# Kernel optimization log

Measured on AMD Instinct MI355X. Metric: run time of the kernel, lower is better.

## Reference

```python
import jax, jax.numpy as jnp
import numpy as np

C_IN, C_KEY, C_VAL, C_OUT = 256, 128, 128, 256
B, H, W = 4, 64, 64
BN_EPS = 1e-5


def conv1x1(x, w, b):
    # x: [B,C,H,W], w: [O,C], b: [O]
    return jnp.einsum('bchw,oc->bohw', x, w) + b[None, :, None, None]


def bn_relu(x, gamma, beta, mean, var):
    inv = jax.lax.rsqrt(var + BN_EPS)
    y = (x - mean[None, :, None, None]) * (gamma * inv)[None, :, None, None] + beta[None, :, None, None]
    return jax.nn.relu(y)


def setup_inputs() -> dict:
    key = jax.random.key(0)
    ks = jax.random.split(key, 16)
    s = 0.05
    return {
        'x_enc': jax.random.normal(ks[0], (B, C_IN, H, W), jnp.float32),
        'x_dec': jax.random.normal(ks[1], (B, C_IN, H, W), jnp.float32),
        # f_key: conv + BN params
        'wk': jax.random.normal(ks[2], (C_KEY, C_IN), jnp.float32) * s,
        'bk': jax.random.normal(ks[3], (C_KEY,), jnp.float32) * s,
        'gk': jax.random.uniform(ks[4], (C_KEY,), jnp.float32, 0.5, 1.5),
        'betak': jax.random.normal(ks[5], (C_KEY,), jnp.float32) * s,
        'mk': jax.random.normal(ks[6], (C_KEY,), jnp.float32) * s,
        'vk': jax.random.uniform(ks[7], (C_KEY,), jnp.float32, 0.5, 1.5),
        # f_query: conv + BN params
        'wq': jax.random.normal(ks[8], (C_KEY, C_IN), jnp.float32) * s,
        'bq': jax.random.normal(ks[9], (C_KEY,), jnp.float32) * s,
        'gq': jax.random.uniform(ks[10], (C_KEY,), jnp.float32, 0.5, 1.5),
        'betaq': jax.random.normal(ks[11], (C_KEY,), jnp.float32) * s,
        'mq': jax.random.normal(ks[12], (C_KEY,), jnp.float32) * s,
        'vq': jax.random.uniform(ks[13], (C_KEY,), jnp.float32, 0.5, 1.5),
        # f_value conv
        'wv': jax.random.normal(ks[14], (C_VAL, C_IN), jnp.float32) * s,
        'bv': jnp.zeros((C_VAL,), jnp.float32),
        # output projection W (random instead of zero-init to avoid degenerate baseline)
        'wo': jax.random.normal(ks[15], (C_OUT, C_VAL), jnp.float32) * s,
        'bo': jnp.zeros((C_OUT,), jnp.float32),
    }


def reference(x_enc, x_dec, wk, bk, gk, betak, mk, vk, wq, bq, gq, betaq, mq, vq, wv, bv, wo, bo):
    b, _, h, w = x_enc.shape
    hw = h * w
    # value: [B, HW, Cv]
    value = conv1x1(x_enc, wv, bv).reshape(b, C_VAL, hw).transpose(0, 2, 1)
    # query: [B, HW, Ck]
    query = bn_relu(conv1x1(x_dec, wq, bq), gq, betaq, mq, vq).reshape(b, C_KEY, hw).transpose(0, 2, 1)
    # key: [B, Ck, HW]
    key = bn_relu(conv1x1(x_enc, wk, bk), gk, betak, mk, vk).reshape(b, C_KEY, hw)
    sim = jnp.einsum('bqc,bck->bqk', query, key) * (C_KEY ** -0.5)  # [B, HW, HW]
    attn = jax.nn.softmax(sim, axis=-1)
    context = jnp.einsum('bqk,bkc->bqc', attn, value)  # [B, HW, Cv]
    context = context.transpose(0, 2, 1).reshape(b, C_VAL, h, w)
    return conv1x1(context, wo, bo)
```

## Files before the change

kernel.cpp:

```cpp
#include <hip/hip_runtime.h>

typedef __attribute__((ext_vector_type(8))) short short8;
typedef __attribute__((ext_vector_type(4))) float floatx4;

#define HW 4096
#define CIN 256
#define CK 128
#define COUT 256
#define NB 4
#define BN_EPS 1e-5f
#define SC2 0.12751744526f

#define MFMA(a, b, c) __builtin_amdgcn_mfma_f32_16x16x32_bf16((a), (b), (c), 0, 0, 0)

__device__ __forceinline__ unsigned short f2bf(float f) {
  union { float f; unsigned u; } v; v.f = f;
  unsigned r = v.u + 0x7fffu + ((v.u >> 16) & 1u);
  return (unsigned short)(r >> 16);
}

__device__ __forceinline__ short8 pack8(const float* p) {
  short8 r;
#pragma unroll
  for (int i = 0; i < 8; ++i) r[i] = (short)f2bf(p[i]);
  return r;
}

__global__ __launch_bounds__(256) void prep_kernel(
    const float* __restrict__ wq, const float* __restrict__ wk,
    const float* __restrict__ wv, const float* __restrict__ wo,
    unsigned short* __restrict__ WqP, unsigned short* __restrict__ WkvP,
    unsigned short* __restrict__ WoP)
{
  const int t = blockIdx.x * 256 + threadIdx.x;
  float tmp[8];
  if (t < 4096) {
    const int lane = t & 63, mt = (t >> 6) & 1, wave = (t >> 7) & 3, ks = t >> 9;
    const int lane16 = lane & 15, quad = lane >> 4;
    const int o = wave * 32 + mt * 16 + lane16;
    const float* src = wq + (size_t)o * CIN + ks * 32 + quad * 8;
    *(float4*)tmp = *(const float4*)src;
    *(float4*)(tmp + 4) = *(const float4*)(src + 4);
    *(short8*)&WqP[(size_t)t * 8] = pack8(tmp);
  } else if (t < 12288) {
    const int u = t - 4096;
    const int lane = u & 63, mt = (u >> 6) & 3, wave = (u >> 8) & 3, ks = u >> 10;
    const int lane16 = lane & 15, quad = lane >> 4;
    const int o = wave * 64 + mt * 16 + lane16;
    const float* row = (o < 128) ? wk + (size_t)o * CIN : wv + (size_t)(o - 128) * CIN;
    const float* src = row + ks * 32 + quad * 8;
    *(float4*)tmp = *(const float4*)src;
    *(float4*)(tmp + 4) = *(const float4*)(src + 4);
    *(short8*)&WkvP[(size_t)u * 8] = pack8(tmp);
  } else {
    const int u = t - 12288;
    const int lane = u & 63, mt = (u >> 6) & 3, wave = (u >> 8) & 3, ks = u >> 10;
    const int lane16 = lane & 15, quad = lane >> 4;
    const int o = wave * 64 + mt * 16 + lane16;
    const float* src = wo + (size_t)o * CK + ks * 32 + quad * 8;
    *(float4*)tmp = *(const float4*)src;
    *(float4*)(tmp + 4) = *(const float4*)(src + 4);
    *(short8*)&WoP[(size_t)u * 8] = pack8(tmp);
  }
}

__global__ __launch_bounds__(256) void proj_kernel(
    const float* __restrict__ x_enc, const float* __restrict__ x_dec,
    const unsigned short* __restrict__ WqP, const unsigned short* __restrict__ WkvP,
    const float* __restrict__ bq, const float* __restrict__ gq,
    const float* __restrict__ betaq, const float* __restrict__ mq,
    const float* __restrict__ vq,
    const float* __restrict__ bk, const float* __restrict__ gk,
    const float* __restrict__ betak, const float* __restrict__ mk,
    const float* __restrict__ vk, const float* __restrict__ bv,
    unsigned short* __restrict__ Qb, unsigned short* __restrict__ Kb,
    unsigned short* __restrict__ Vt)
{
  const int tid = threadIdx.x;
  const int pt = blockIdx.x;
  const int b  = blockIdx.y;
  const int pj = blockIdx.z;

  const float* X = (pj == 0) ? x_dec : x_enc;

  __shared__ float xF[64 * 68];
  __shared__ unsigned short xT[64 * 264];

  const float* Xs = X + (size_t)b * CIN * HW + (size_t)pt * 64;
#pragma unroll
  for (int qtr = 0; qtr < 4; ++qtr) {
    if (qtr) __syncthreads();
    {
      const int c = tid >> 2;
      const int p0 = (tid & 3) * 16;
      const float* src = Xs + (size_t)(qtr * 64 + c) * HW + p0;
#pragma unroll
      for (int j = 0; j < 4; ++j)
        *(float4*)&xF[c * 68 + p0 + j * 4] = *(const float4*)(src + j * 4);
    }
    __syncthreads();
    {
      const int p = tid & 63;
      const int cb = tid >> 6;
#pragma unroll
      for (int jj = 0; jj < 2; ++jj) {
        const int c0 = (jj * 4 + cb) * 8;
        float t[8];
#pragma unroll
        for (int u = 0; u < 8; ++u) t[u] = xF[(c0 + u) * 68 + p];
        *(short8*)&xT[p * 264 + qtr * 64 + c0] = pack8(t);
      }
    }
  }
  __syncthreads();

  const int wave = tid >> 6;
  const int lane = tid & 63;
  const int lane16 = lane & 15;
  const int quad = lane >> 4;

  if (pj == 0) {
    floatx4 acc[2][4];
#pragma unroll
    for (int mt = 0; mt < 2; ++mt)
#pragma unroll
      for (int nf = 0; nf < 4; ++nf) acc[mt][nf] = (floatx4){0.f, 0.f, 0.f, 0.f};

#pragma unroll
    for (int ks = 0; ks < 8; ++ks) {
      short8 af[2];
#pragma unroll
      for (int mt = 0; mt < 2; ++mt)
        af[mt] = *(const short8*)&WqP[(size_t)((((ks * 4 + wave) * 2 + mt) * 64) + lane) * 8];
#pragma unroll
      for (int nf = 0; nf < 4; ++nf) {
        const short8 bf = *(const short8*)&xT[(nf * 16 + lane16) * 264 + ks * 32 + quad * 8];
#pragma unroll
        for (int mt = 0; mt < 2; ++mt) acc[mt][nf] = MFMA(af[mt], bf, acc[mt][nf]);
      }
    }

    float sc[2][4], off[2][4];
#pragma unroll
    for (int mt = 0; mt < 2; ++mt)
#pragma unroll
      for (int r = 0; r < 4; ++r) {
        const int o = wave * 32 + mt * 16 + quad * 4 + r;
        const float s = gq[o] * rsqrtf(vq[o] + BN_EPS) * SC2;
        sc[mt][r] = s;
        off[mt][r] = (bq[o] - mq[o]) * s + betaq[o] * SC2;
      }
#pragma unroll
    for (int nf = 0; nf < 4; ++nf) {
      const size_t prow = ((size_t)b * HW + pt * 64 + nf * 16 + lane16) * CK;
#pragma unroll
      for (int mt = 0; mt < 2; ++mt) {
        ushort4 pk;
        pk.x = f2bf(fmaxf(acc[mt][nf][0] * sc[mt][0] + off[mt][0], 0.f));
        pk.y = f2bf(fmaxf(acc[mt][nf][1] * sc[mt][1] + off[mt][1], 0.f));
        pk.z = f2bf(fmaxf(acc[mt][nf][2] * sc[mt][2] + off[mt][2], 0.f));
        pk.w = f2bf(fmaxf(acc[mt][nf][3] * sc[mt][3] + off[mt][3], 0.f));
        *(ushort4*)(Qb + prow + wave * 32 + mt * 16 + quad * 4) = pk;
      }
    }
  } else {
    const bool isK = (wave < 2);
    floatx4 acc[4][4];
#pragma unroll
    for (int mt = 0; mt < 4; ++mt)
#pragma unroll
      for (int nf = 0; nf < 4; ++nf) acc[mt][nf] = (floatx4){0.f, 0.f, 0.f, 0.f};

#pragma unroll
    for (int ks = 0; ks < 8; ++ks) {
      short8 af[4];
#pragma unroll
      for (int mt = 0; mt < 4; ++mt)
        af[mt] = *(const short8*)&WkvP[(size_t)((((ks * 4 + wave) * 4 + mt) * 64) + lane) * 8];
#pragma unroll
      for (int nf = 0; nf < 4; ++nf) {
        const short8 bf = *(const short8*)&xT[(nf * 16 + lane16) * 264 + ks * 32 + quad * 8];
#pragma unroll
        for (int mt = 0; mt < 4; ++mt) acc[mt][nf] = MFMA(af[mt], bf, acc[mt][nf]);
      }
    }

    if (isK) {
      float sc[4][4], off[4][4];
#pragma unroll
      for (int mt = 0; mt < 4; ++mt)
#pragma unroll
        for (int r = 0; r < 4; ++r) {
          const int o = wave * 64 + mt * 16 + quad * 4 + r;
          const float s = gk[o] * rsqrtf(vk[o] + BN_EPS);
          sc[mt][r] = s;
          off[mt][r] = (bk[o] - mk[o]) * s + betak[o];
        }
#pragma unroll
      for (int nf = 0; nf < 4; ++nf) {
        const size_t prow = ((size_t)b * HW + pt * 64 + nf * 16 + lane16) * CK;
#pragma unroll
        for (int mt = 0; mt < 4; ++mt) {
          ushort4 pk;
          pk.x = f2bf(fmaxf(acc[mt][nf][0] * sc[mt][0] + off[mt][0], 0.f));
          pk.y = f2bf(fmaxf(acc[mt][nf][1] * sc[mt][1] + off[mt][1], 0.f));
          pk.z = f2bf(fmaxf(acc[mt][nf][2] * sc[mt][2] + off[mt][2], 0.f));
          pk.w = f2bf(fmaxf(acc[mt][nf][3] * sc[mt][3] + off[mt][3], 0.f));
          *(ushort4*)(Kb + prow + wave * 64 + mt * 16 + quad * 4) = pk;
        }
      }
    } else {
#pragma unroll
      for (int mt = 0; mt < 4; ++mt) {
#pragma unroll
        for (int r = 0; r < 4; ++r) {
          const int c = wave * 64 + mt * 16 + quad * 4 + r - 128;
          const float bias = bv[c];
          unsigned short* dst = Vt + ((size_t)(b * CK + c)) * HW + pt * 64;
#pragma unroll
          for (int nf = 0; nf < 4; ++nf)
            dst[nf * 16 + lane16] = f2bf(acc[mt][nf][r] + bias);
        }
      }
    }
  }
}

template<int NKC>
__global__ __launch_bounds__(256, 2) void attn_kernel5(
    const unsigned short* __restrict__ Qb, const unsigned short* __restrict__ Kb,
    const unsigned short* __restrict__ Vt, float* __restrict__ Opart,
    float* __restrict__ Ml)
{
  constexpr int ITERS = 64 / NKC;
  const int tid = threadIdx.x;
  const int blk = blockIdx.x;
  const int b  = blk & 3;
  const int qt = (blk >> 2) & 31;
  const int kc = blk >> 7;

  const int wave = tid >> 6;
  const int lane = tid & 63;
  const int lane16 = lane & 15;
  const int quad = lane >> 4;

  __shared__ unsigned short Kl[64 * 136];
  __shared__ unsigned short Vl[128 * 72];
  __shared__ unsigned short Pl[4][32 * 72];
  unsigned short* Pw = &Pl[wave][0];

  const int q0 = qt * 128 + wave * 32;
  short8 qf[2][4];
  {
    const unsigned short* Qs = Qb + ((size_t)b * HW + q0) * CK;
#pragma unroll
    for (int mt = 0; mt < 2; ++mt)
#pragma unroll
      for (int ks = 0; ks < 4; ++ks)
        qf[mt][ks] = *(const short8*)(Qs + (size_t)(mt * 16 + lane16) * CK + ks * 32 + quad * 8);
  }

  short8 ones;
#pragma unroll
  for (int i = 0; i < 8; ++i) ones[i] = (short)0x3F80;

  floatx4 O[2][8];
  floatx4 Lacc[2];
#pragma unroll
  for (int mt = 0; mt < 2; ++mt) {
    Lacc[mt] = (floatx4){0.f, 0.f, 0.f, 0.f};
#pragma unroll
    for (int nf = 0; nf < 8; ++nf) O[mt][nf] = (floatx4){0.f, 0.f, 0.f, 0.f};
  }

  const int krow = tid >> 4;
  const int kcol = (tid & 15) * 8;
  const int vrow = tid >> 1;
  const int vcol = (tid & 1) * 32;

  const unsigned short* Kg = Kb + (size_t)b * HW * CK + (size_t)(kc * ITERS * 64) * CK;
  const unsigned short* Vg = Vt + (size_t)b * CK * HW + kc * ITERS * 64;

  short8 kr[4], vr[4];
#pragma unroll
  for (int i2 = 0; i2 < 4; ++i2)
    kr[i2] = *(const short8*)(Kg + (size_t)(krow + i2 * 16) * CK + kcol);
#pragma unroll
  for (int i2 = 0; i2 < 4; ++i2)
    vr[i2] = *(const short8*)(Vg + (size_t)vrow * HW + vcol + i2 * 8);

  for (int it = 0; it < ITERS; ++it) {
    __syncthreads();
#pragma unroll
    for (int i2 = 0; i2 < 4; ++i2)
      *(short8*)&Kl[(krow + i2 * 16) * 136 + kcol] = kr[i2];
#pragma unroll
    for (int i2 = 0; i2 < 4; ++i2)
      *(short8*)&Vl[vrow * 72 + vcol + i2 * 8] = vr[i2];
    __syncthreads();

    if (it + 1 < ITERS) {
      const unsigned short* Kn = Kg + (size_t)((it + 1) * 64) * CK;
      const unsigned short* Vn = Vg + (it + 1) * 64;
#pragma unroll
      for (int i2 = 0; i2 < 4; ++i2)
        kr[i2] = *(const short8*)(Kn + (size_t)(krow + i2 * 16) * CK + kcol);
#pragma unroll
      for (int i2 = 0; i2 < 4; ++i2)
        vr[i2] = *(const short8*)(Vn + (size_t)vrow * HW + vcol + i2 * 8);
    }

#pragma unroll
    for (int nf = 0; nf < 4; ++nf) {
      floatx4 s0 = (floatx4){0.f, 0.f, 0.f, 0.f};
      floatx4 s1 = (floatx4){0.f, 0.f, 0.f, 0.f};
#pragma unroll
      for (int ks = 0; ks < 4; ++ks) {
        const short8 kf = *(const short8*)&Kl[(nf * 16 + lane16) * 136 + ks * 32 + quad * 8];
        s0 = MFMA(qf[0][ks], kf, s0);
        s1 = MFMA(qf[1][ks], kf, s1);
      }
#pragma unroll
      for (int r = 0; r < 4; ++r) {
        Pw[(quad * 4 + r) * 72 + nf * 16 + lane16] =
            f2bf(__builtin_amdgcn_exp2f(s0[r]));
        Pw[(16 + quad * 4 + r) * 72 + nf * 16 + lane16] =
            f2bf(__builtin_amdgcn_exp2f(s1[r]));
      }
    }
    __threadfence_block();

#pragma unroll
    for (int ks = 0; ks < 2; ++ks) {
      const short8 pf0 = *(const short8*)&Pw[lane16 * 72 + ks * 32 + quad * 8];
      const short8 pf1 = *(const short8*)&Pw[(16 + lane16) * 72 + ks * 32 + quad * 8];
      Lacc[0] = MFMA(pf0, ones, Lacc[0]);
      Lacc[1] = MFMA(pf1, ones, Lacc[1]);
#pragma unroll
      for (int nf = 0; nf < 8; ++nf) {
        const short8 vf = *(const short8*)&Vl[(nf * 16 + lane16) * 72 + ks * 32 + quad * 8];
        O[0][nf] = MFMA(pf0, vf, O[0][nf]);
        O[1][nf] = MFMA(pf1, vf, O[1][nf]);
      }
    }
  }

  const int chunk = (b * 32 + qt) * NKC + kc;
  float* Op = Opart + (size_t)chunk * (128 * 128);
#pragma unroll
  for (int mt = 0; mt < 2; ++mt)
#pragma unroll
    for (int nf = 0; nf < 8; ++nf)
#pragma unroll
      for (int r = 0; r < 4; ++r)
        Op[(size_t)(wave * 32 + mt * 16 + quad * 4 + r) * 128 + nf * 16 + lane16] = O[mt][nf][r];
  if (lane16 == 0) {
    float* Mp = Ml + (size_t)chunk * 128 + wave * 32;
#pragma unroll
    for (int mt = 0; mt < 2; ++mt)
#pragma unroll
      for (int r = 0; r < 4; ++r)
        Mp[mt * 16 + quad * 4 + r] = Lacc[mt][r];
  }
}

template<int NKC>
__global__ __launch_bounds__(256) void outproj_kernel(
    const float* __restrict__ Opart, const float* __restrict__ Ml,
    const unsigned short* __restrict__ WoP, const float* __restrict__ bo,
    float* __restrict__ out)
{
  const int tid = threadIdx.x;
  const int pt = blockIdx.x;
  const int b  = blockIdx.y;
  const int qt = pt >> 3;
  const int q0 = (pt & 7) * 16;
  const int chunk0 = (b * 32 + qt) * NKC;

  __shared__ unsigned short Ctile[16 * 136];

  {
    const int row = tid >> 4;
    const int c8  = (tid & 15) * 8;
    float L = 0.f;
#pragma unroll
    for (int k = 0; k < NKC; ++k) L += Ml[(size_t)(chunk0 + k) * 128 + q0 + row];
    float acc[8];
#pragma unroll
    for (int i = 0; i < 8; ++i) acc[i] = 0.f;
#pragma unroll
    for (int k = 0; k < NKC; ++k) {
      const float* Op = Opart + (size_t)(chunk0 + k) * 16384 + (size_t)(q0 + row) * 128 + c8;
      const float4 v0 = *(const float4*)(Op);
      const float4 v1 = *(const float4*)(Op + 4);
      acc[0] += v0.x; acc[1] += v0.y; acc[2] += v0.z; acc[3] += v0.w;
      acc[4] += v1.x; acc[5] += v1.y; acc[6] += v1.z; acc[7] += v1.w;
    }
    const float inv = 1.f / L;
#pragma unroll
    for (int i = 0; i < 8; ++i) acc[i] *= inv;
    *(short8*)&Ctile[row * 136 + c8] = pack8(acc);
  }
  __syncthreads();

  const int wave = tid >> 6;
  const int lane = tid & 63;
  const int lane16 = lane & 15;
  const int quad = lane >> 4;

  floatx4 acc[4];
#pragma unroll
  for (int mt = 0; mt < 4; ++mt) acc[mt] = (floatx4){0.f, 0.f, 0.f, 0.f};

#pragma unroll
  for (int ks = 0; ks < 4; ++ks) {
    const short8 bf = *(const short8*)&Ctile[lane16 * 136 + ks * 32 + quad * 8];
#pragma unroll
    for (int mt = 0; mt < 4; ++mt) {
      const short8 af = *(const short8*)&WoP[(size_t)((((ks * 4 + wave) * 4 + mt) * 64) + lane) * 8];
      acc[mt] = MFMA(af, bf, acc[mt]);
    }
  }

#pragma unroll
  for (int mt = 0; mt < 4; ++mt) {
#pragma unroll
    for (int r = 0; r < 4; ++r) {
      const int o = wave * 64 + mt * 16 + quad * 4 + r;
      float* dst = out + ((size_t)b * COUT + o) * HW + qt * 128 + q0;
      dst[lane16] = acc[mt][r] + bo[o];
    }
  }
}

extern "C" void kernel_launch(void* const* d_in, const int* in_sizes, int n_in,
                              void* d_out, int out_size, void* d_ws, size_t ws_size,
                              hipStream_t stream)
{
  (void)in_sizes; (void)n_in; (void)out_size;
  const float* x_enc = (const float*)d_in[0];
  const float* x_dec = (const float*)d_in[1];
  const float* wk    = (const float*)d_in[2];
  const float* bk    = (const float*)d_in[3];
  const float* gk    = (const float*)d_in[4];
  const float* betak = (const float*)d_in[5];
  const float* mk    = (const float*)d_in[6];
  const float* vk    = (const float*)d_in[7];
  const float* wq    = (const float*)d_in[8];
  const float* bq    = (const float*)d_in[9];
  const float* gq    = (const float*)d_in[10];
  const float* betaq = (const float*)d_in[11];
  const float* mq    = (const float*)d_in[12];
  const float* vq    = (const float*)d_in[13];
  const float* wv    = (const float*)d_in[14];
  const float* bv    = (const float*)d_in[15];
  const float* wo    = (const float*)d_in[16];
  const float* bo    = (const float*)d_in[17];
  float* out = (float*)d_out;

  const size_t qkv = (size_t)NB * HW * CK;
  unsigned short* WqP  = (unsigned short*)d_ws;
  unsigned short* WkvP = WqP + 32768;
  unsigned short* WoP  = WkvP + 65536;
  unsigned short* Qb   = WoP + 32768;
  unsigned short* Kb   = Qb + qkv;
  unsigned short* Vt   = Kb + qkv;
  float* Opart = (float*)(Vt + qkv);
  const size_t fixed_bytes = 131072 * 2 + 3 * qkv * 2;

  prep_kernel<<<dim3(64), 256, 0, stream>>>(wq, wk, wv, wo, WqP, WkvP, WoP);
  proj_kernel<<<dim3(64, 4, 2), 256, 0, stream>>>(
      x_enc, x_dec, WqP, WkvP,
      bq, gq, betaq, mq, vq, bk, gk, betak, mk, vk, bv, Qb, Kb, Vt);

  auto need = [&](int nkc) {
    return fixed_bytes + (size_t)128 * nkc * (16384 + 128) * sizeof(float);
  };
  if (ws_size >= need(8)) {
    float* Ml = Opart + (size_t)128 * 8 * 16384;
    attn_kernel5<8><<<dim3(1024), 256, 0, stream>>>(Qb, Kb, Vt, Opart, Ml);
    outproj_kernel<8><<<dim3(256, 4), 256, 0, stream>>>(Opart, Ml, WoP, bo, out);
  } else if (ws_size >= need(4)) {
    float* Ml = Opart + (size_t)128 * 4 * 16384;
    attn_kernel5<4><<<dim3(512), 256, 0, stream>>>(Qb, Kb, Vt, Opart, Ml);
    outproj_kernel<4><<<dim3(256, 4), 256, 0, stream>>>(Opart, Ml, WoP, bo, out);
  } else if (ws_size >= need(2)) {
    float* Ml = Opart + (size_t)128 * 2 * 16384;
    attn_kernel5<2><<<dim3(256), 256, 0, stream>>>(Qb, Kb, Vt, Opart, Ml);
    outproj_kernel<2><<<dim3(256, 4), 256, 0, stream>>>(Opart, Ml, WoP, bo, out);
  } else {
    float* Ml = Opart + (size_t)128 * 1 * 16384;
    attn_kernel5<1><<<dim3(128), 256, 0, stream>>>(Qb, Kb, Vt, Opart, Ml);
    outproj_kernel<1><<<dim3(256, 4), 256, 0, stream>>>(Opart, Ml, WoP, bo, out);
  }
}
```

Before: 177.4 us.

## Double attention query tile per block to 256 rows, 64 per wave

Each wave of the attention kernel now handles 64 query rows instead of 32, so a block covers 256 queries. Every K and V tile loaded into shared memory is reused across twice as many queries, and the P tile is processed in two 32-key halves to keep shared memory small. The partial-output layout and the outproj indexing change to match. The cost is twice as many accumulator registers per wave, which puts occupancy at two blocks per CU at risk, and half as many blocks in the grid.

```diff
diff --git a/kernel.cpp b/kernel.cpp
--- a/kernel.cpp
+++ b/kernel.cpp
@@ -227,7 +227,7 @@
 }
 
 template<int NKC>
-__global__ __launch_bounds__(256, 2) void attn_kernel5(
+__global__ __launch_bounds__(256, 2) void attn_kernel7(
     const unsigned short* __restrict__ Qb, const unsigned short* __restrict__ Kb,
     const unsigned short* __restrict__ Vt, float* __restrict__ Opart,
     float* __restrict__ Ml)
@@ -236,8 +236,8 @@
   const int tid = threadIdx.x;
   const int blk = blockIdx.x;
   const int b  = blk & 3;
-  const int qt = (blk >> 2) & 31;
-  const int kc = blk >> 7;
+  const int qt = (blk >> 2) & 15;
+  const int kc = blk >> 6;
 
   const int wave = tid >> 6;
   const int lane = tid & 63;
@@ -246,15 +246,15 @@
 
   __shared__ unsigned short Kl[64 * 136];
   __shared__ unsigned short Vl[128 * 72];
-  __shared__ unsigned short Pl[4][32 * 72];
+  __shared__ unsigned short Pl[4][64 * 40];
   unsigned short* Pw = &Pl[wave][0];
 
-  const int q0 = qt * 128 + wave * 32;
-  short8 qf[2][4];
+  const int q0 = qt * 256 + wave * 64;
+  short8 qf[4][4];
   {
     const unsigned short* Qs = Qb + ((size_t)b * HW + q0) * CK;
 #pragma unroll
-    for (int mt = 0; mt < 2; ++mt)
+    for (int mt = 0; mt < 4; ++mt)
 #pragma unroll
       for (int ks = 0; ks < 4; ++ks)
         qf[mt][ks] = *(const short8*)(Qs + (size_t)(mt * 16 + lane16) * CK + ks * 32 + quad * 8);
@@ -264,10 +264,10 @@
 #pragma unroll
   for (int i = 0; i < 8; ++i) ones[i] = (short)0x3F80;
 
-  floatx4 O[2][8];
-  floatx4 Lacc[2];
-#pragma unroll
-  for (int mt = 0; mt < 2; ++mt) {
+  floatx4 O[4][8];
+  floatx4 Lacc[4];
+#pragma unroll
+  for (int mt = 0; mt < 4; ++mt) {
     Lacc[mt] = (floatx4){0.f, 0.f, 0.f, 0.f};
 #pragma unroll
     for (int nf = 0; nf < 8; ++nf) O[mt][nf] = (floatx4){0.f, 0.f, 0.f, 0.f};
@@ -311,53 +311,56 @@
     }
 
 #pragma unroll
-    for (int nf = 0; nf < 4; ++nf) {
-      floatx4 s0 = (floatx4){0.f, 0.f, 0.f, 0.f};
-      floatx4 s1 = (floatx4){0.f, 0.f, 0.f, 0.f};
-#pragma unroll
-      for (int ks = 0; ks < 4; ++ks) {
-        const short8 kf = *(const short8*)&Kl[(nf * 16 + lane16) * 136 + ks * 32 + quad * 8];
-        s0 = MFMA(qf[0][ks], kf, s0);
-        s1 = MFMA(qf[1][ks], kf, s1);
-      }
-#pragma unroll
-      for (int r = 0; r < 4; ++r) {
-        Pw[(quad * 4 + r) * 72 + nf * 16 + lane16] =
-            f2bf(__builtin_amdgcn_exp2f(s0[r]));
-        Pw[(16 + quad * 4 + r) * 72 + nf * 16 + lane16] =
-            f2bf(__builtin_amdgcn_exp2f(s1[r]));
-      }
-    }
-    __threadfence_block();
-
-#pragma unroll
-    for (int ks = 0; ks < 2; ++ks) {
-      const short8 pf0 = *(const short8*)&Pw[lane16 * 72 + ks * 32 + quad * 8];
-      const short8 pf1 = *(const short8*)&Pw[(16 + lane16) * 72 + ks * 32 + quad * 8];
-      Lacc[0] = MFMA(pf0, ones, Lacc[0]);
-      Lacc[1] = MFMA(pf1, ones, Lacc[1]);
+    for (int h = 0; h < 2; ++h) {
+#pragma unroll
+      for (int nfl = 0; nfl < 2; ++nfl) {
+        floatx4 s[4];
+#pragma unroll
+        for (int mt = 0; mt < 4; ++mt) s[mt] = (floatx4){0.f, 0.f, 0.f, 0.f};
+#pragma unroll
+        for (int ks = 0; ks < 4; ++ks) {
+          const short8 kf = *(const short8*)&Kl[(h * 32 + nfl * 16 + lane16) * 136 + ks * 32 + quad * 8];
+#pragma unroll
+          for (int mt = 0; mt < 4; ++mt) s[mt] = MFMA(qf[mt][ks], kf, s[mt]);
+        }
+#pragma unroll
+        for (int mt = 0; mt < 4; ++mt)
+#pragma unroll
+          for (int r = 0; r < 4; ++r)
+            Pw[(mt * 16 + quad * 4 + r) * 40 + nfl * 16 + lane16] =
+                f2bf(__builtin_amdgcn_exp2f(s[mt][r]));
+      }
+      __threadfence_block();
+
+      short8 pf[4];
+#pragma unroll
+      for (int mt = 0; mt < 4; ++mt) {
+        pf[mt] = *(const short8*)&Pw[(mt * 16 + lane16) * 40 + quad * 8];
+        Lacc[mt] = MFMA(pf[mt], ones, Lacc[mt]);
+      }
 #pragma unroll
       for (int nf = 0; nf < 8; ++nf) {
-        const short8 vf = *(const short8*)&Vl[(nf * 16 + lane16) * 72 + ks * 32 + quad * 8];
-        O[0][nf] = MFMA(pf0, vf, O[0][nf]);
-        O[1][nf] = MFMA(pf1, vf, O[1][nf]);
-      }
-    }
-  }
-
-  const int chunk = (b * 32 + qt) * NKC + kc;
-  float* Op = Opart + (size_t)chunk * (128 * 128);
-#pragma unroll
-  for (int mt = 0; mt < 2; ++mt)
+        const short8 vf = *(const short8*)&Vl[(nf * 16 + lane16) * 72 + h * 32 + quad * 8];
+#pragma unroll
+        for (int mt = 0; mt < 4; ++mt) O[mt][nf] = MFMA(pf[mt], vf, O[mt][nf]);
+      }
+      __threadfence_block();
+    }
+  }
+
+  const int chunk = (b * 16 + qt) * NKC + kc;
+  float* Op = Opart + (size_t)chunk * (256 * 128);
+#pragma unroll
+  for (int mt = 0; mt < 4; ++mt)
 #pragma unroll
     for (int nf = 0; nf < 8; ++nf)
 #pragma unroll
       for (int r = 0; r < 4; ++r)
-        Op[(size_t)(wave * 32 + mt * 16 + quad * 4 + r) * 128 + nf * 16 + lane16] = O[mt][nf][r];
+        Op[(size_t)(wave * 64 + mt * 16 + quad * 4 + r) * 128 + nf * 16 + lane16] = O[mt][nf][r];
   if (lane16 == 0) {
-    float* Mp = Ml + (size_t)chunk * 128 + wave * 32;
-#pragma unroll
-    for (int mt = 0; mt < 2; ++mt)
+    float* Mp = Ml + (size_t)chunk * 256 + wave * 64;
+#pragma unroll
+    for (int mt = 0; mt < 4; ++mt)
 #pragma unroll
       for (int r = 0; r < 4; ++r)
         Mp[mt * 16 + quad * 4 + r] = Lacc[mt][r];
@@ -373,9 +376,9 @@
   const int tid = threadIdx.x;
   const int pt = blockIdx.x;
   const int b  = blockIdx.y;
-  const int qt = pt >> 3;
-  const int q0 = (pt & 7) * 16;
-  const int chunk0 = (b * 32 + qt) * NKC;
+  const int qt  = pt >> 4;
+  const int qin = (pt & 15) * 16;
+  const int chunk0 = (b * 16 + qt) * NKC;
 
   __shared__ unsigned short Ctile[16 * 136];
 
@@ -384,13 +387,13 @@
     const int c8  = (tid & 15) * 8;
     float L = 0.f;
 #pragma unroll
-    for (int k = 0; k < NKC; ++k) L += Ml[(size_t)(chunk0 + k) * 128 + q0 + row];
+    for (int k = 0; k < NKC; ++k) L += Ml[(size_t)(chunk0 + k) * 256 + qin + row];
     float acc[8];
 #pragma unroll
     for (int i = 0; i < 8; ++i) acc[i] = 0.f;
 #pragma unroll
     for (int k = 0; k < NKC; ++k) {
-      const float* Op = Opart + (size_t)(chunk0 + k) * 16384 + (size_t)(q0 + row) * 128 + c8;
+      const float* Op = Opart + (size_t)(chunk0 + k) * 32768 + (size_t)(qin + row) * 128 + c8;
       const float4 v0 = *(const float4*)(Op);
       const float4 v1 = *(const float4*)(Op + 4);
       acc[0] += v0.x; acc[1] += v0.y; acc[2] += v0.z; acc[3] += v0.w;
@@ -427,7 +430,7 @@
 #pragma unroll
     for (int r = 0; r < 4; ++r) {
       const int o = wave * 64 + mt * 16 + quad * 4 + r;
-      float* dst = out + ((size_t)b * COUT + o) * HW + qt * 128 + q0;
+      float* dst = out + ((size_t)b * COUT + o) * HW + qt * 256 + qin;
       dst[lane16] = acc[mt][r] + bo[o];
     }
   }
@@ -474,23 +477,23 @@
       bq, gq, betaq, mq, vq, bk, gk, betak, mk, vk, bv, Qb, Kb, Vt);
 
   auto need = [&](int nkc) {
-    return fixed_bytes + (size_t)128 * nkc * (16384 + 128) * sizeof(float);
+    return fixed_bytes + (size_t)64 * nkc * (32768 + 256) * sizeof(float);
   };
   if (ws_size >= need(8)) {
-    float* Ml = Opart + (size_t)128 * 8 * 16384;
-    attn_kernel5<8><<<dim3(1024), 256, 0, stream>>>(Qb, Kb, Vt, Opart, Ml);
+    float* Ml = Opart + (size_t)64 * 8 * 32768;
+    attn_kernel7<8><<<dim3(512), 256, 0, stream>>>(Qb, Kb, Vt, Opart, Ml);
     outproj_kernel<8><<<dim3(256, 4), 256, 0, stream>>>(Opart, Ml, WoP, bo, out);
   } else if (ws_size >= need(4)) {
-    float* Ml = Opart + (size_t)128 * 4 * 16384;
-    attn_kernel5<4><<<dim3(512), 256, 0, stream>>>(Qb, Kb, Vt, Opart, Ml);
+    float* Ml = Opart + (size_t)64 * 4 * 32768;
+    attn_kernel7<4><<<dim3(256), 256, 0, stream>>>(Qb, Kb, Vt, Opart, Ml);
     outproj_kernel<4><<<dim3(256, 4), 256, 0, stream>>>(Opart, Ml, WoP, bo, out);
   } else if (ws_size >= need(2)) {
-    float* Ml = Opart + (size_t)128 * 2 * 16384;
-    attn_kernel5<2><<<dim3(256), 256, 0, stream>>>(Qb, Kb, Vt, Opart, Ml);
+    float* Ml = Opart + (size_t)64 * 2 * 32768;
+    attn_kernel7<2><<<dim3(128), 256, 0, stream>>>(Qb, Kb, Vt, Opart, Ml);
     outproj_kernel<2><<<dim3(256, 4), 256, 0, stream>>>(Opart, Ml, WoP, bo, out);
   } else {
-    float* Ml = Opart + (size_t)128 * 1 * 16384;
-    attn_kernel5<1><<<dim3(128), 256, 0, stream>>>(Qb, Kb, Vt, Opart, Ml);
+    float* Ml = Opart + (size_t)64 * 1 * 32768;
+    attn_kernel7<1><<<dim3(64), 256, 0, stream>>>(Qb, Kb, Vt, Opart, Ml);
     outproj_kernel<1><<<dim3(256, 4), 256, 0, stream>>>(Opart, Ml, WoP, bo, out);
   }
 }
```

Result: slower. 191.3 us (+7.9%).
